# Optimization experiments

Hardware: AMD Instinct MI355X
Metric: run time of the kernel (lower is better)

Reference implementation:

```python
import jax, jax.numpy as jnp
import numpy as np

ALPHA = 0.1
K = 5


def setup_inputs() -> dict:
    key = jax.random.key(0)
    ks = jax.random.split(key, 6)
    N, E = 50000, 800000
    IN, HID, OUT = 512, 256, 64
    x = jax.random.normal(ks[0], (N, IN), dtype=jnp.float32)
    edge_index = jax.random.randint(ks[1], (2, E), 0, N, dtype=jnp.int64)
    # Linear params (torch Linear: y = x @ W.T + b), kaiming-ish scale
    W1 = jax.random.normal(ks[2], (HID, IN), dtype=jnp.float32) / np.sqrt(IN)
    b1 = jnp.zeros((HID,), dtype=jnp.float32)
    W2 = jax.random.normal(ks[3], (OUT, HID), dtype=jnp.float32) / np.sqrt(HID)
    b2 = jnp.zeros((OUT,), dtype=jnp.float32)
    return {"x": x, "W1": W1, "b1": b1, "W2": W2, "b2": b2,
            "edge_index": edge_index}


def reference(x, W1, b1, W2, b2, edge_index):
    N = x.shape[0]
    # --- MLP encoder (eval mode: dropout is identity) ---
    h = jax.nn.relu(x @ W1.T + b1)          # [N, HID]
    h = h @ W2.T + b2                       # [N, OUT]

    # --- gcn_norm with self-loops (PyG APPNP default) ---
    src, dst = edge_index[0], edge_index[1]
    loop = jnp.arange(N, dtype=src.dtype)
    src_f = jnp.concatenate([src, loop])    # [E+N]
    dst_f = jnp.concatenate([dst, loop])
    ew = jnp.ones(src_f.shape[0], dtype=h.dtype)
    deg = jax.ops.segment_sum(ew, dst_f, num_segments=N)
    dinv = jnp.where(deg > 0, jax.lax.rsqrt(deg), 0.0)
    norm = dinv[src_f] * dinv[dst_f]        # [E+N]

    # --- K iterations of personalized-PageRank propagation ---
    def body(xk, _):
        msg = norm[:, None] * xk[src_f]                      # gather [E+N, OUT]
        agg = jax.ops.segment_sum(msg, dst_f, num_segments=N)
        return (1.0 - ALPHA) * agg + ALPHA * h, None

    xK, _ = jax.lax.scan(body, h, None, length=K)
    return jax.nn.log_softmax(xK, axis=1)
```

## Files before the change

kernel.cpp:

```cpp
#include <hip/hip_runtime.h>
#include <hip/hip_bf16.h>

#define IN_DIM  512
#define HID_DIM 256
#define OUT_DIM 64

typedef __attribute__((ext_vector_type(8))) short bf16x8;
typedef __attribute__((ext_vector_type(4))) float f32x4;

static __device__ __forceinline__ ushort f2b(float f) {
    __hip_bfloat16 b = __float2bfloat16(f);
    return *reinterpret_cast<ushort*>(&b);
}
static __device__ __forceinline__ float b2f_lo(uint u) {
    union { uint u; float f; } t; t.u = u << 16; return t.f;
}
static __device__ __forceinline__ float b2f_hi(uint u) {
    union { uint u; float f; } t; t.u = u & 0xFFFF0000u; return t.f;
}
static __device__ __forceinline__ uint packbf(float x, float y) {
    return (uint)f2b(x) | ((uint)f2b(y) << 16);
}


__global__ void hist_kernel(const int* __restrict__ ei, int* __restrict__ deg, int E) {
    int e = blockIdx.x * 256 + threadIdx.x;
    if (e < E) atomicAdd(&deg[ei[E + e]], 1);
}

__global__ __launch_bounds__(256) void scanA_kernel(const int* __restrict__ deg,
                                                    int* __restrict__ offs,
                                                    int* __restrict__ bsum, int N) {
    __shared__ int sh[256];
    int tid = threadIdx.x;
    int i = blockIdx.x * 256 + tid;
    int v = (i < N) ? deg[i] : 0;
    sh[tid] = v;
    __syncthreads();
#pragma unroll
    for (int off = 1; off < 256; off <<= 1) {
        int t = (tid >= off) ? sh[tid - off] : 0;
        __syncthreads();
        sh[tid] += t;
        __syncthreads();
    }
    if (i < N) offs[i] = sh[tid] - v;
    if (tid == 255) bsum[blockIdx.x] = sh[255];
}

__global__ __launch_bounds__(256) void scanB_kernel(int* __restrict__ bsum, int nb) {
    __shared__ int sh[256];
    int tid = threadIdx.x;
    int v = (tid < nb) ? bsum[tid] : 0;
    sh[tid] = v;
    __syncthreads();
#pragma unroll
    for (int off = 1; off < 256; off <<= 1) {
        int t = (tid >= off) ? sh[tid - off] : 0;
        __syncthreads();
        sh[tid] += t;
        __syncthreads();
    }
    if (tid < nb) bsum[tid] = sh[tid] - v;
}

__global__ __launch_bounds__(256) void scanC_kernel(const int* __restrict__ deg,
                                                    const int* __restrict__ bsum,
                                                    int* __restrict__ offs,
                                                    float* __restrict__ dinv,
                                                    int N, int E) {
    int i = blockIdx.x * 256 + threadIdx.x;
    if (i < N) {
        offs[i] += bsum[i >> 8];
        dinv[i] = rsqrtf((float)(deg[i] + 1));
    }
    if (i == 0) offs[N] = E;
}

__global__ void fill_kernel(const int* __restrict__ ei, const int* __restrict__ offs,
                            int* __restrict__ cursor, const float* __restrict__ dinv,
                            uint* __restrict__ edat, int E) {
    int e = blockIdx.x * 256 + threadIdx.x;
    if (e < E) {
        int s = ei[e];
        int d = ei[E + e];
        int pos = offs[d] + atomicAdd(&cursor[d], 1);
        edat[pos] = (uint)s | ((uint)f2b(dinv[d] * dinv[s]) << 16);
    }
}


__global__ __launch_bounds__(512, 4) void gemm1_bres(const float* __restrict__ A,
                                                     const float* __restrict__ W1,
                                                     const float* __restrict__ bias,
                                                     ushort* __restrict__ C, int M) {
    constexpr int K = IN_DIM;
    constexpr int NK = K / 32;
    __shared__ ushort Bs[64 * 512];

    const int tid  = threadIdx.x;
    const int lane = tid & 63;
    const int w    = tid >> 6;
    const int n0 = blockIdx.x * 64;
    const int m0 = blockIdx.y * 256;
    const int l15 = lane & 15;
    const int lq  = lane >> 4;

    {
        const int c = tid >> 3;
        const int gb = (tid & 7) * 8;
#pragma unroll
        for (int i = 0; i < 8; ++i) {
            const int g = gb + i;
            const float* src = W1 + (size_t)(n0 + c) * K + g * 8;
            float4 v0 = *reinterpret_cast<const float4*>(src);
            float4 v1 = *reinterpret_cast<const float4*>(src + 4);
            ushort4 u0 = make_ushort4(f2b(v0.x), f2b(v0.y), f2b(v0.z), f2b(v0.w));
            ushort4 u1 = make_ushort4(f2b(v1.x), f2b(v1.y), f2b(v1.z), f2b(v1.w));
            ushort* dst = &Bs[c * 512 + (g ^ (c & 7)) * 8];
            *reinterpret_cast<ushort4*>(dst)     = u0;
            *reinterpret_cast<ushort4*>(dst + 4) = u1;
        }
    }
    __syncthreads();

    const int r0 = m0 + w * 32;
    const int koff = lq * 8;

    int arow0 = r0 + l15;      if (arow0 >= M) arow0 = M - 1;
    int arow1 = r0 + 16 + l15; if (arow1 >= M) arow1 = M - 1;
    const float* ga0 = A + (size_t)arow0 * K + koff;
    const float* ga1 = A + (size_t)arow1 * K + koff;

    f32x4 acc[2][4];
#pragma unroll
    for (int i = 0; i < 2; ++i)
#pragma unroll
        for (int j = 0; j < 4; ++j) acc[i][j] = (f32x4)0.0f;

    float4 pv[2][2];
    pv[0][0] = *reinterpret_cast<const float4*>(ga0);
    pv[0][1] = *reinterpret_cast<const float4*>(ga0 + 4);
    pv[1][0] = *reinterpret_cast<const float4*>(ga1);
    pv[1][1] = *reinterpret_cast<const float4*>(ga1 + 4);

    for (int ks = 0; ks < NK; ++ks) {
        float4 cv[2][2];
#pragma unroll
        for (int rf = 0; rf < 2; ++rf) { cv[rf][0] = pv[rf][0]; cv[rf][1] = pv[rf][1]; }
        if (ks + 1 < NK) {
            const int k1 = (ks + 1) * 32;
            pv[0][0] = *reinterpret_cast<const float4*>(ga0 + k1);
            pv[0][1] = *reinterpret_cast<const float4*>(ga0 + k1 + 4);
            pv[1][0] = *reinterpret_cast<const float4*>(ga1 + k1);
            pv[1][1] = *reinterpret_cast<const float4*>(ga1 + k1 + 4);
        }
        bf16x8 af[2];
#pragma unroll
        for (int rf = 0; rf < 2; ++rf) {
            bf16x8 a;
            a[0] = (short)f2b(cv[rf][0].x); a[1] = (short)f2b(cv[rf][0].y);
            a[2] = (short)f2b(cv[rf][0].z); a[3] = (short)f2b(cv[rf][0].w);
            a[4] = (short)f2b(cv[rf][1].x); a[5] = (short)f2b(cv[rf][1].y);
            a[6] = (short)f2b(cv[rf][1].z); a[7] = (short)f2b(cv[rf][1].w);
            af[rf] = a;
        }
        bf16x8 bf[4];
#pragma unroll
        for (int cf = 0; cf < 4; ++cf) {
            const int c = cf * 16 + l15;
            const int g = ks * 4 + lq;
            bf[cf] = *reinterpret_cast<const bf16x8*>(&Bs[c * 512 + (g ^ (c & 7)) * 8]);
        }
#pragma unroll
        for (int rf = 0; rf < 2; ++rf)
#pragma unroll
            for (int cf = 0; cf < 4; ++cf)
                acc[rf][cf] = __builtin_amdgcn_mfma_f32_16x16x32_bf16(af[rf], bf[cf], acc[rf][cf], 0, 0, 0);
    }

    const int lr = lq * 4;
#pragma unroll
    for (int cf = 0; cf < 4; ++cf) {
        int col = n0 + cf * 16 + l15;
        float bv = bias[col];
#pragma unroll
        for (int rf = 0; rf < 2; ++rf) {
#pragma unroll
            for (int j = 0; j < 4; ++j) {
                int row = r0 + rf * 16 + lr + j;
                if (row < M) {
                    float v = fmaxf(acc[rf][cf][j] + bv, 0.f);
                    C[(size_t)row * HID_DIM + col] = f2b(v);
                }
            }
        }
    }
}


#define LDT 40

__global__ __launch_bounds__(256) void gemm2_bf16(const ushort* __restrict__ A,
                                                  const float* __restrict__ B,
                                                  const float* __restrict__ bias,
                                                  ushort* __restrict__ Cb,
                                                  int M) {
    constexpr int K = HID_DIM;
    constexpr int NK = K / 32;
    __shared__ ushort As[128 * LDT];
    __shared__ ushort Bs[64 * LDT];

    const int tid = threadIdx.x;
    const int lane = tid & 63;
    const int wid = tid >> 6;
    const int wm = wid >> 1, wn = wid & 1;
    const int m0 = blockIdx.x * 128;
    const int l15 = lane & 15;
    const int koff = (lane >> 4) * 8;

    f32x4 acc[4][2];
#pragma unroll
    for (int i = 0; i < 4; ++i)
#pragma unroll
        for (int j = 0; j < 2; ++j) acc[i][j] = (f32x4)0.0f;

    uint4 rawA[2];
    float4 rbv[2];
#pragma unroll
    for (int i = 0; i < 2; ++i) {
        int slot = tid + i * 256;
        int rowA = slot >> 2, c8 = (slot & 3) << 3;
        int m = m0 + rowA;
        rawA[i] = (m < M) ? *reinterpret_cast<const uint4*>(&A[(size_t)m * K + c8])
                          : make_uint4(0u, 0u, 0u, 0u);
        int rowB = slot >> 3, c4 = (slot & 7) << 2;
        rbv[i] = *reinterpret_cast<const float4*>(&B[(size_t)rowB * K + c4]);
    }
#pragma unroll
    for (int i = 0; i < 2; ++i) {
        int slot = tid + i * 256;
        int rowA = slot >> 2, c8 = (slot & 3) << 3;
        *reinterpret_cast<uint4*>(&As[rowA * LDT + c8]) = rawA[i];
        int rowB = slot >> 3, c4 = (slot & 7) << 2;
        ushort4 ub = make_ushort4(f2b(rbv[i].x), f2b(rbv[i].y), f2b(rbv[i].z), f2b(rbv[i].w));
        *reinterpret_cast<ushort4*>(&Bs[rowB * LDT + c4]) = ub;
    }
    __syncthreads();

    for (int ks = 0; ks < NK; ++ks) {
        if (ks + 1 < NK) {
            int k0 = (ks + 1) * 32;
#pragma unroll
            for (int i = 0; i < 2; ++i) {
                int slot = tid + i * 256;
                int rowA = slot >> 2, c8 = (slot & 3) << 3;
                int m = m0 + rowA;
                rawA[i] = (m < M) ? *reinterpret_cast<const uint4*>(&A[(size_t)m * K + k0 + c8])
                                  : make_uint4(0u, 0u, 0u, 0u);
                int rowB = slot >> 3, c4 = (slot & 7) << 2;
                rbv[i] = *reinterpret_cast<const float4*>(&B[(size_t)rowB * K + k0 + c4]);
            }
        }
        bf16x8 af[4], bf[2];
#pragma unroll
        for (int f = 0; f < 4; ++f)
            af[f] = *reinterpret_cast<const bf16x8*>(&As[(wm * 64 + f * 16 + l15) * LDT + koff]);
#pragma unroll
        for (int f = 0; f < 2; ++f)
            bf[f] = *reinterpret_cast<const bf16x8*>(&Bs[(wn * 32 + f * 16 + l15) * LDT + koff]);
#pragma unroll
        for (int i = 0; i < 4; ++i)
#pragma unroll
            for (int j = 0; j < 2; ++j)
                acc[i][j] = __builtin_amdgcn_mfma_f32_16x16x32_bf16(af[i], bf[j], acc[i][j], 0, 0, 0);
        __syncthreads();
        if (ks + 1 < NK) {
#pragma unroll
            for (int i = 0; i < 2; ++i) {
                int slot = tid + i * 256;
                int rowA = slot >> 2, c8 = (slot & 3) << 3;
                *reinterpret_cast<uint4*>(&As[rowA * LDT + c8]) = rawA[i];
                int rowB = slot >> 3, c4 = (slot & 7) << 2;
                ushort4 ub = make_ushort4(f2b(rbv[i].x), f2b(rbv[i].y), f2b(rbv[i].z), f2b(rbv[i].w));
                *reinterpret_cast<ushort4*>(&Bs[rowB * LDT + c4]) = ub;
            }
            __syncthreads();
        }
    }

    const int lr = (lane >> 4) * 4;
#pragma unroll
    for (int nf = 0; nf < 2; ++nf) {
        int col = wn * 32 + nf * 16 + l15;
        float bv = bias[col];
#pragma unroll
        for (int mf = 0; mf < 4; ++mf) {
#pragma unroll
            for (int j = 0; j < 4; ++j) {
                int row = m0 + wm * 64 + mf * 16 + lr + j;
                if (row < M)
                    Cb[(size_t)row * OUT_DIM + col] = f2b(acc[mf][nf][j] + bv);
            }
        }
    }
}


__global__ __launch_bounds__(256) void propb_kernel(const uint* __restrict__ xin,
                                                    const uint* __restrict__ hb,
                                                    const float* __restrict__ dinv,
                                                    const int* __restrict__ offs,
                                                    const uint* __restrict__ edat,
                                                    uint* __restrict__ xout, int N) {
    int node = blockIdx.x * 8 + (threadIdx.x >> 5);
    int l32 = threadIdx.x & 31;
    if (node >= N) return;
    int e0 = offs[node], e1 = offs[node + 1];

    float ax[4] = {0.f, 0.f, 0.f, 0.f};
    float ay[4] = {0.f, 0.f, 0.f, 0.f};
    int e = e0;
    for (; e + 8 <= e1; e += 8) {
        uint p0 = edat[e+0], p1 = edat[e+1], p2 = edat[e+2], p3 = edat[e+3];
        uint p4 = edat[e+4], p5 = edat[e+5], p6 = edat[e+6], p7 = edat[e+7];
        uint g0 = xin[(size_t)(p0 & 0xFFFFu) * 32 + l32];
        uint g1 = xin[(size_t)(p1 & 0xFFFFu) * 32 + l32];
        uint g2 = xin[(size_t)(p2 & 0xFFFFu) * 32 + l32];
        uint g3 = xin[(size_t)(p3 & 0xFFFFu) * 32 + l32];
        uint g4 = xin[(size_t)(p4 & 0xFFFFu) * 32 + l32];
        uint g5 = xin[(size_t)(p5 & 0xFFFFu) * 32 + l32];
        uint g6 = xin[(size_t)(p6 & 0xFFFFu) * 32 + l32];
        uint g7 = xin[(size_t)(p7 & 0xFFFFu) * 32 + l32];
        ax[0] = fmaf(b2f_hi(p0), b2f_lo(g0), ax[0]); ay[0] = fmaf(b2f_hi(p0), b2f_hi(g0), ay[0]);
        ax[1] = fmaf(b2f_hi(p1), b2f_lo(g1), ax[1]); ay[1] = fmaf(b2f_hi(p1), b2f_hi(g1), ay[1]);
        ax[2] = fmaf(b2f_hi(p2), b2f_lo(g2), ax[2]); ay[2] = fmaf(b2f_hi(p2), b2f_hi(g2), ay[2]);
        ax[3] = fmaf(b2f_hi(p3), b2f_lo(g3), ax[3]); ay[3] = fmaf(b2f_hi(p3), b2f_hi(g3), ay[3]);
        ax[0] = fmaf(b2f_hi(p4), b2f_lo(g4), ax[0]); ay[0] = fmaf(b2f_hi(p4), b2f_hi(g4), ay[0]);
        ax[1] = fmaf(b2f_hi(p5), b2f_lo(g5), ax[1]); ay[1] = fmaf(b2f_hi(p5), b2f_hi(g5), ay[1]);
        ax[2] = fmaf(b2f_hi(p6), b2f_lo(g6), ax[2]); ay[2] = fmaf(b2f_hi(p6), b2f_hi(g6), ay[2]);
        ax[3] = fmaf(b2f_hi(p7), b2f_lo(g7), ax[3]); ay[3] = fmaf(b2f_hi(p7), b2f_hi(g7), ay[3]);
    }
    for (; e < e1; ++e) {
        uint p = edat[e];
        uint g = xin[(size_t)(p & 0xFFFFu) * 32 + l32];
        ax[0] = fmaf(b2f_hi(p), b2f_lo(g), ax[0]);
        ay[0] = fmaf(b2f_hi(p), b2f_hi(g), ay[0]);
    }
    float sx = (ax[0] + ax[1]) + (ax[2] + ax[3]);
    float sy = (ay[0] + ay[1]) + (ay[2] + ay[3]);
    float di = dinv[node];
    uint gs = xin[(size_t)node * 32 + l32];
    sx = fmaf(di * di, b2f_lo(gs), sx);
    sy = fmaf(di * di, b2f_hi(gs), sy);
    uint ah = hb[(size_t)node * 32 + l32];
    float r0 = 0.9f * sx + 0.1f * b2f_lo(ah);
    float r1 = 0.9f * sy + 0.1f * b2f_hi(ah);
    xout[(size_t)node * 32 + l32] = packbf(r0, r1);
}


__global__ __launch_bounds__(256) void propb_lsm_kernel(const uint* __restrict__ xin,
                                                        const uint* __restrict__ hb,
                                                        const float* __restrict__ dinv,
                                                        const int* __restrict__ offs,
                                                        const uint* __restrict__ edat,
                                                        float* __restrict__ out, int N) {
    int node = blockIdx.x * 8 + (threadIdx.x >> 5);
    int l32 = threadIdx.x & 31;
    if (node >= N) return;
    int e0 = offs[node], e1 = offs[node + 1];

    float ax[4] = {0.f, 0.f, 0.f, 0.f};
    float ay[4] = {0.f, 0.f, 0.f, 0.f};
    int e = e0;
    for (; e + 8 <= e1; e += 8) {
        uint p0 = edat[e+0], p1 = edat[e+1], p2 = edat[e+2], p3 = edat[e+3];
        uint p4 = edat[e+4], p5 = edat[e+5], p6 = edat[e+6], p7 = edat[e+7];
        uint g0 = xin[(size_t)(p0 & 0xFFFFu) * 32 + l32];
        uint g1 = xin[(size_t)(p1 & 0xFFFFu) * 32 + l32];
        uint g2 = xin[(size_t)(p2 & 0xFFFFu) * 32 + l32];
        uint g3 = xin[(size_t)(p3 & 0xFFFFu) * 32 + l32];
        uint g4 = xin[(size_t)(p4 & 0xFFFFu) * 32 + l32];
        uint g5 = xin[(size_t)(p5 & 0xFFFFu) * 32 + l32];
        uint g6 = xin[(size_t)(p6 & 0xFFFFu) * 32 + l32];
        uint g7 = xin[(size_t)(p7 & 0xFFFFu) * 32 + l32];
        ax[0] = fmaf(b2f_hi(p0), b2f_lo(g0), ax[0]); ay[0] = fmaf(b2f_hi(p0), b2f_hi(g0), ay[0]);
        ax[1] = fmaf(b2f_hi(p1), b2f_lo(g1), ax[1]); ay[1] = fmaf(b2f_hi(p1), b2f_hi(g1), ay[1]);
        ax[2] = fmaf(b2f_hi(p2), b2f_lo(g2), ax[2]); ay[2] = fmaf(b2f_hi(p2), b2f_hi(g2), ay[2]);
        ax[3] = fmaf(b2f_hi(p3), b2f_lo(g3), ax[3]); ay[3] = fmaf(b2f_hi(p3), b2f_hi(g3), ay[3]);
        ax[0] = fmaf(b2f_hi(p4), b2f_lo(g4), ax[0]); ay[0] = fmaf(b2f_hi(p4), b2f_hi(g4), ay[0]);
        ax[1] = fmaf(b2f_hi(p5), b2f_lo(g5), ax[1]); ay[1] = fmaf(b2f_hi(p5), b2f_hi(g5), ay[1]);
        ax[2] = fmaf(b2f_hi(p6), b2f_lo(g6), ax[2]); ay[2] = fmaf(b2f_hi(p6), b2f_hi(g6), ay[2]);
        ax[3] = fmaf(b2f_hi(p7), b2f_lo(g7), ax[3]); ay[3] = fmaf(b2f_hi(p7), b2f_hi(g7), ay[3]);
    }
    for (; e < e1; ++e) {
        uint p = edat[e];
        uint g = xin[(size_t)(p & 0xFFFFu) * 32 + l32];
        ax[0] = fmaf(b2f_hi(p), b2f_lo(g), ax[0]);
        ay[0] = fmaf(b2f_hi(p), b2f_hi(g), ay[0]);
    }
    float sx = (ax[0] + ax[1]) + (ax[2] + ax[3]);
    float sy = (ay[0] + ay[1]) + (ay[2] + ay[3]);
    float di = dinv[node];
    uint gs = xin[(size_t)node * 32 + l32];
    sx = fmaf(di * di, b2f_lo(gs), sx);
    sy = fmaf(di * di, b2f_hi(gs), sy);
    uint ah = hb[(size_t)node * 32 + l32];
    float r0 = 0.9f * sx + 0.1f * b2f_lo(ah);
    float r1 = 0.9f * sy + 0.1f * b2f_hi(ah);

    float m = fmaxf(r0, r1);
    for (int o = 16; o > 0; o >>= 1) m = fmaxf(m, __shfl_xor(m, o));
    float sum = expf(r0 - m) + expf(r1 - m);
    for (int o = 16; o > 0; o >>= 1) sum += __shfl_xor(sum, o);
    float ls = logf(sum);
    float2 o2 = make_float2(r0 - m - ls, r1 - m - ls);
    *reinterpret_cast<float2*>(&out[(size_t)node * 64 + l32 * 2]) = o2;
}


static inline size_t align256(size_t x) { return (x + 255) & ~(size_t)255; }

extern "C" void kernel_launch(void* const* d_in, const int* in_sizes, int n_in,
                              void* d_out, int out_size, void* d_ws, size_t ws_size,
                              hipStream_t stream) {
    const float* x  = (const float*)d_in[0];
    const float* W1 = (const float*)d_in[1];
    const float* b1 = (const float*)d_in[2];
    const float* W2 = (const float*)d_in[3];
    const float* b2 = (const float*)d_in[4];
    const int*   ei = (const int*)d_in[5];

    const int N = in_sizes[0] / IN_DIM;
    const int E = in_sizes[5] / 2;
    const int nb = (N + 255) / 256;

    char* base = (char*)d_ws;
    size_t off = 0;
    uint*  hb  = (uint*)(base + off);    off += align256((size_t)N * 32 * 4);
    uint*  xsa = (uint*)(base + off);    off += align256((size_t)N * 32 * 4);
    uint*  xsb = (uint*)(base + off);    off += align256((size_t)N * 32 * 4);
    ushort* h1  = (ushort*)(base + off); off += align256((size_t)N * HID_DIM * 2);
    float* dinv = (float*)(base + off);  off += align256((size_t)N * 4);
    int*   deg  = (int*)(base + off);    off += align256((size_t)N * 4);
    int*   offs = (int*)(base + off);    off += align256((size_t)(N + 1) * 4);
    int*   cur  = (int*)(base + off);    off += align256((size_t)N * 4);
    int*   bsum = (int*)(base + off);    off += align256((size_t)nb * 4);
    uint*  edat = (uint*)(base + off);   off += align256((size_t)E * 4);

    hipMemsetAsync(deg, 0, (size_t)N * 4, stream);
    hipMemsetAsync(cur, 0, (size_t)N * 4, stream);
    hist_kernel<<<(E + 255) / 256, 256, 0, stream>>>(ei, deg, E);
    scanA_kernel<<<nb, 256, 0, stream>>>(deg, offs, bsum, N);
    scanB_kernel<<<1, 256, 0, stream>>>(bsum, nb);
    scanC_kernel<<<nb, 256, 0, stream>>>(deg, bsum, offs, dinv, N, E);
    fill_kernel<<<(E + 255) / 256, 256, 0, stream>>>(ei, offs, cur, dinv, edat, E);

    {
        dim3 g(4, (N + 255) / 256);
        gemm1_bres<<<g, 512, 0, stream>>>(x, W1, b1, h1, N);
    }
    {
        dim3 g((N + 127) / 128);
        gemm2_bf16<<<g, 256, 0, stream>>>(h1, W2, b2, (ushort*)hb, N);
    }

    int blocks = (N + 7) / 8;
    propb_kernel<<<blocks, 256, 0, stream>>>(hb,  hb, dinv, offs, edat, xsa, N);
    propb_kernel<<<blocks, 256, 0, stream>>>(xsa, hb, dinv, offs, edat, xsb, N);
    propb_kernel<<<blocks, 256, 0, stream>>>(xsb, hb, dinv, offs, edat, xsa, N);
    propb_kernel<<<blocks, 256, 0, stream>>>(xsa, hb, dinv, offs, edat, xsb, N);
    propb_lsm_kernel<<<blocks, 256, 0, stream>>>(xsb, hb, dinv, offs, edat,
                                                 (float*)d_out, N);
}
```

Measured before the change: 324.4 us.

## Deepen GEMM prefetch to three stages, pad LDS, and unroll propagation gathers

The first GEMM now prefetches A tiles three K-steps ahead in a rotating register buffer and fully unrolls the K loop. The B tile in LDS uses a padded row stride instead of an XOR swizzle to avoid bank conflicts. The propagation kernels gather 16 neighbour rows per iteration, with a 4-wide remainder loop, to keep more loads in flight. The changes trade extra registers, which can lower occupancy, and slightly more LDS for better latency hiding in these memory-bound loops.

```diff
diff --git a/kernel.cpp b/kernel.cpp
--- a/kernel.cpp
+++ b/kernel.cpp
@@ -90,13 +90,15 @@
 }
 
 
+#define BSTR 520
+
 __global__ __launch_bounds__(512, 4) void gemm1_bres(const float* __restrict__ A,
                                                      const float* __restrict__ W1,
                                                      const float* __restrict__ bias,
                                                      ushort* __restrict__ C, int M) {
     constexpr int K = IN_DIM;
     constexpr int NK = K / 32;
-    __shared__ ushort Bs[64 * 512];
+    __shared__ ushort Bs[64 * BSTR];
 
     const int tid  = threadIdx.x;
     const int lane = tid & 63;
@@ -117,7 +119,7 @@
             float4 v1 = *reinterpret_cast<const float4*>(src + 4);
             ushort4 u0 = make_ushort4(f2b(v0.x), f2b(v0.y), f2b(v0.z), f2b(v0.w));
             ushort4 u1 = make_ushort4(f2b(v1.x), f2b(v1.y), f2b(v1.z), f2b(v1.w));
-            ushort* dst = &Bs[c * 512 + (g ^ (c & 7)) * 8];
+            ushort* dst = &Bs[c * BSTR + g * 8];
             *reinterpret_cast<ushort4*>(dst)     = u0;
             *reinterpret_cast<ushort4*>(dst + 4) = u1;
         }
@@ -138,39 +140,41 @@
 #pragma unroll
         for (int j = 0; j < 4; ++j) acc[i][j] = (f32x4)0.0f;
 
-    float4 pv[2][2];
-    pv[0][0] = *reinterpret_cast<const float4*>(ga0);
-    pv[0][1] = *reinterpret_cast<const float4*>(ga0 + 4);
-    pv[1][0] = *reinterpret_cast<const float4*>(ga1);
-    pv[1][1] = *reinterpret_cast<const float4*>(ga1 + 4);
-
+    float4 pv[3][2][2];
+#pragma unroll
+    for (int d = 0; d < 3; ++d) {
+        const int k1 = d * 32;
+        pv[d][0][0] = *reinterpret_cast<const float4*>(ga0 + k1);
+        pv[d][0][1] = *reinterpret_cast<const float4*>(ga0 + k1 + 4);
+        pv[d][1][0] = *reinterpret_cast<const float4*>(ga1 + k1);
+        pv[d][1][1] = *reinterpret_cast<const float4*>(ga1 + k1 + 4);
+    }
+
+#pragma unroll
     for (int ks = 0; ks < NK; ++ks) {
-        float4 cv[2][2];
-#pragma unroll
-        for (int rf = 0; rf < 2; ++rf) { cv[rf][0] = pv[rf][0]; cv[rf][1] = pv[rf][1]; }
-        if (ks + 1 < NK) {
-            const int k1 = (ks + 1) * 32;
-            pv[0][0] = *reinterpret_cast<const float4*>(ga0 + k1);
-            pv[0][1] = *reinterpret_cast<const float4*>(ga0 + k1 + 4);
-            pv[1][0] = *reinterpret_cast<const float4*>(ga1 + k1);
-            pv[1][1] = *reinterpret_cast<const float4*>(ga1 + k1 + 4);
-        }
+        const int slot = ks % 3;
         bf16x8 af[2];
 #pragma unroll
         for (int rf = 0; rf < 2; ++rf) {
             bf16x8 a;
-            a[0] = (short)f2b(cv[rf][0].x); a[1] = (short)f2b(cv[rf][0].y);
-            a[2] = (short)f2b(cv[rf][0].z); a[3] = (short)f2b(cv[rf][0].w);
-            a[4] = (short)f2b(cv[rf][1].x); a[5] = (short)f2b(cv[rf][1].y);
-            a[6] = (short)f2b(cv[rf][1].z); a[7] = (short)f2b(cv[rf][1].w);
+            a[0] = (short)f2b(pv[slot][rf][0].x); a[1] = (short)f2b(pv[slot][rf][0].y);
+            a[2] = (short)f2b(pv[slot][rf][0].z); a[3] = (short)f2b(pv[slot][rf][0].w);
+            a[4] = (short)f2b(pv[slot][rf][1].x); a[5] = (short)f2b(pv[slot][rf][1].y);
+            a[6] = (short)f2b(pv[slot][rf][1].z); a[7] = (short)f2b(pv[slot][rf][1].w);
             af[rf] = a;
+        }
+        if (ks + 3 < NK) {
+            const int k1 = (ks + 3) * 32;
+            pv[slot][0][0] = *reinterpret_cast<const float4*>(ga0 + k1);
+            pv[slot][0][1] = *reinterpret_cast<const float4*>(ga0 + k1 + 4);
+            pv[slot][1][0] = *reinterpret_cast<const float4*>(ga1 + k1);
+            pv[slot][1][1] = *reinterpret_cast<const float4*>(ga1 + k1 + 4);
         }
         bf16x8 bf[4];
 #pragma unroll
         for (int cf = 0; cf < 4; ++cf) {
             const int c = cf * 16 + l15;
-            const int g = ks * 4 + lq;
-            bf[cf] = *reinterpret_cast<const bf16x8*>(&Bs[c * 512 + (g ^ (c & 7)) * 8]);
+            bf[cf] = *reinterpret_cast<const bf16x8*>(&Bs[c * BSTR + (ks * 4 + lq) * 8]);
         }
 #pragma unroll
         for (int rf = 0; rf < 2; ++rf)
@@ -321,25 +325,31 @@
     float ax[4] = {0.f, 0.f, 0.f, 0.f};
     float ay[4] = {0.f, 0.f, 0.f, 0.f};
     int e = e0;
-    for (; e + 8 <= e1; e += 8) {
-        uint p0 = edat[e+0], p1 = edat[e+1], p2 = edat[e+2], p3 = edat[e+3];
-        uint p4 = edat[e+4], p5 = edat[e+5], p6 = edat[e+6], p7 = edat[e+7];
-        uint g0 = xin[(size_t)(p0 & 0xFFFFu) * 32 + l32];
-        uint g1 = xin[(size_t)(p1 & 0xFFFFu) * 32 + l32];
-        uint g2 = xin[(size_t)(p2 & 0xFFFFu) * 32 + l32];
-        uint g3 = xin[(size_t)(p3 & 0xFFFFu) * 32 + l32];
-        uint g4 = xin[(size_t)(p4 & 0xFFFFu) * 32 + l32];
-        uint g5 = xin[(size_t)(p5 & 0xFFFFu) * 32 + l32];
-        uint g6 = xin[(size_t)(p6 & 0xFFFFu) * 32 + l32];
-        uint g7 = xin[(size_t)(p7 & 0xFFFFu) * 32 + l32];
-        ax[0] = fmaf(b2f_hi(p0), b2f_lo(g0), ax[0]); ay[0] = fmaf(b2f_hi(p0), b2f_hi(g0), ay[0]);
-        ax[1] = fmaf(b2f_hi(p1), b2f_lo(g1), ax[1]); ay[1] = fmaf(b2f_hi(p1), b2f_hi(g1), ay[1]);
-        ax[2] = fmaf(b2f_hi(p2), b2f_lo(g2), ax[2]); ay[2] = fmaf(b2f_hi(p2), b2f_hi(g2), ay[2]);
-        ax[3] = fmaf(b2f_hi(p3), b2f_lo(g3), ax[3]); ay[3] = fmaf(b2f_hi(p3), b2f_hi(g3), ay[3]);
-        ax[0] = fmaf(b2f_hi(p4), b2f_lo(g4), ax[0]); ay[0] = fmaf(b2f_hi(p4), b2f_hi(g4), ay[0]);
-        ax[1] = fmaf(b2f_hi(p5), b2f_lo(g5), ax[1]); ay[1] = fmaf(b2f_hi(p5), b2f_hi(g5), ay[1]);
-        ax[2] = fmaf(b2f_hi(p6), b2f_lo(g6), ax[2]); ay[2] = fmaf(b2f_hi(p6), b2f_hi(g6), ay[2]);
-        ax[3] = fmaf(b2f_hi(p7), b2f_lo(g7), ax[3]); ay[3] = fmaf(b2f_hi(p7), b2f_hi(g7), ay[3]);
+    for (; e + 16 <= e1; e += 16) {
+        uint p[16], g[16];
+#pragma unroll
+        for (int i = 0; i < 16; ++i) p[i] = edat[e + i];
+#pragma unroll
+        for (int i = 0; i < 16; ++i) g[i] = xin[(size_t)(p[i] & 0xFFFFu) * 32 + l32];
+#pragma unroll
+        for (int i = 0; i < 16; ++i) {
+            float wgt = b2f_hi(p[i]);
+            ax[i & 3] = fmaf(wgt, b2f_lo(g[i]), ax[i & 3]);
+            ay[i & 3] = fmaf(wgt, b2f_hi(g[i]), ay[i & 3]);
+        }
+    }
+    for (; e + 4 <= e1; e += 4) {
+        uint p[4], g[4];
+#pragma unroll
+        for (int i = 0; i < 4; ++i) p[i] = edat[e + i];
+#pragma unroll
+        for (int i = 0; i < 4; ++i) g[i] = xin[(size_t)(p[i] & 0xFFFFu) * 32 + l32];
+#pragma unroll
+        for (int i = 0; i < 4; ++i) {
+            float wgt = b2f_hi(p[i]);
+            ax[i] = fmaf(wgt, b2f_lo(g[i]), ax[i]);
+            ay[i] = fmaf(wgt, b2f_hi(g[i]), ay[i]);
+        }
     }
     for (; e < e1; ++e) {
         uint p = edat[e];
@@ -374,25 +384,31 @@
     float ax[4] = {0.f, 0.f, 0.f, 0.f};
     float ay[4] = {0.f, 0.f, 0.f, 0.f};
     int e = e0;
-    for (; e + 8 <= e1; e += 8) {
-        uint p0 = edat[e+0], p1 = edat[e+1], p2 = edat[e+2], p3 = edat[e+3];
-        uint p4 = edat[e+4], p5 = edat[e+5], p6 = edat[e+6], p7 = edat[e+7];
-        uint g0 = xin[(size_t)(p0 & 0xFFFFu) * 32 + l32];
-        uint g1 = xin[(size_t)(p1 & 0xFFFFu) * 32 + l32];
-        uint g2 = xin[(size_t)(p2 & 0xFFFFu) * 32 + l32];
-        uint g3 = xin[(size_t)(p3 & 0xFFFFu) * 32 + l32];
-        uint g4 = xin[(size_t)(p4 & 0xFFFFu) * 32 + l32];
-        uint g5 = xin[(size_t)(p5 & 0xFFFFu) * 32 + l32];
-        uint g6 = xin[(size_t)(p6 & 0xFFFFu) * 32 + l32];
-        uint g7 = xin[(size_t)(p7 & 0xFFFFu) * 32 + l32];
-        ax[0] = fmaf(b2f_hi(p0), b2f_lo(g0), ax[0]); ay[0] = fmaf(b2f_hi(p0), b2f_hi(g0), ay[0]);
-        ax[1] = fmaf(b2f_hi(p1), b2f_lo(g1), ax[1]); ay[1] = fmaf(b2f_hi(p1), b2f_hi(g1), ay[1]);
-        ax[2] = fmaf(b2f_hi(p2), b2f_lo(g2), ax[2]); ay[2] = fmaf(b2f_hi(p2), b2f_hi(g2), ay[2]);
-        ax[3] = fmaf(b2f_hi(p3), b2f_lo(g3), ax[3]); ay[3] = fmaf(b2f_hi(p3), b2f_hi(g3), ay[3]);
-        ax[0] = fmaf(b2f_hi(p4), b2f_lo(g4), ax[0]); ay[0] = fmaf(b2f_hi(p4), b2f_hi(g4), ay[0]);
-        ax[1] = fmaf(b2f_hi(p5), b2f_lo(g5), ax[1]); ay[1] = fmaf(b2f_hi(p5), b2f_hi(g5), ay[1]);
-        ax[2] = fmaf(b2f_hi(p6), b2f_lo(g6), ax[2]); ay[2] = fmaf(b2f_hi(p6), b2f_hi(g6), ay[2]);
-        ax[3] = fmaf(b2f_hi(p7), b2f_lo(g7), ax[3]); ay[3] = fmaf(b2f_hi(p7), b2f_hi(g7), ay[3]);
+    for (; e + 16 <= e1; e += 16) {
+        uint p[16], g[16];
+#pragma unroll
+        for (int i = 0; i < 16; ++i) p[i] = edat[e + i];
+#pragma unroll
+        for (int i = 0; i < 16; ++i) g[i] = xin[(size_t)(p[i] & 0xFFFFu) * 32 + l32];
+#pragma unroll
+        for (int i = 0; i < 16; ++i) {
+            float wgt = b2f_hi(p[i]);
+            ax[i & 3] = fmaf(wgt, b2f_lo(g[i]), ax[i & 3]);
+            ay[i & 3] = fmaf(wgt, b2f_hi(g[i]), ay[i & 3]);
+        }
+    }
+    for (; e + 4 <= e1; e += 4) {
+        uint p[4], g[4];
+#pragma unroll
+        for (int i = 0; i < 4; ++i) p[i] = edat[e + i];
+#pragma unroll
+        for (int i = 0; i < 4; ++i) g[i] = xin[(size_t)(p[i] & 0xFFFFu) * 32 + l32];
+#pragma unroll
+        for (int i = 0; i < 4; ++i) {
+            float wgt = b2f_hi(p[i]);
+            ax[i] = fmaf(wgt, b2f_lo(g[i]), ax[i]);
+            ay[i] = fmaf(wgt, b2f_hi(g[i]), ay[i]);
+        }
     }
     for (; e < e1; ++e) {
         uint p = edat[e];
```

Measured after the change: 312.7 us. 3.6% less time.
